# Kernel optimization log

Measured on AMD Instinct MI355X. Metric: run time of the kernel, lower is better.

Reference implementation:

```python
import jax, jax.numpy as jnp
import numpy as np

N = 50000   # nodes
E = 800000  # edges
D = 96      # feature dim


def setup_inputs() -> dict:
    key = jax.random.key(0)
    k1, k2, k3, k4 = jax.random.split(key, 4)
    scale = 1.0 / np.sqrt(D)
    return {
        "x": jax.random.normal(k1, (N, D), dtype=jnp.float32),
        "edge_index": jax.random.randint(k2, (2, E), 0, N, dtype=jnp.int64),
        "W1": jax.random.normal(k3, (D, D), dtype=jnp.float32) * scale,
        "b1": jnp.zeros((D,), dtype=jnp.float32),
        "W2": jax.random.normal(k4, (D, D), dtype=jnp.float32) * scale,
        "b2": jnp.zeros((D,), dtype=jnp.float32),
    }


def _gcn_conv(x, src, dst, W, b, n_nodes):
    # PyG GCNConv: linear transform, add self-loops, symmetric normalization,
    # scatter-add aggregation from src (row) to dst (col), then bias.
    h = x @ W  # [N, D_out]
    loops = jnp.arange(n_nodes, dtype=src.dtype)
    s = jnp.concatenate([src, loops])  # [E+N]
    d = jnp.concatenate([dst, loops])  # [E+N]
    deg = jax.ops.segment_sum(jnp.ones_like(d, dtype=h.dtype), d, num_segments=n_nodes)
    dinv = jnp.where(deg > 0, jax.lax.rsqrt(deg), 0.0)  # deg^-1/2, 0 for isolated
    norm = dinv[s] * dinv[d]  # [E+N]
    msg = norm[:, None] * h[s]  # gather + scale
    out = jax.ops.segment_sum(msg, d, num_segments=n_nodes)  # scatter-add
    return out + b


def reference(x, edge_index, W1, b1, W2, b2):
    src, dst = edge_index[0], edge_index[1]
    # dropout p=0.0 -> identity. ReLU after every layer (loop break never fires).
    h = _gcn_conv(x, src, dst, W1, b1, N)
    h = jax.nn.relu(h)
    h = _gcn_conv(h, src, dst, W2, b2, N)
    h = jax.nn.relu(h)
    return h
```

## Files before the change

kernel.cpp:

```cpp
#include <hip/hip_runtime.h>
#include <hip/hip_fp16.h>

#define NN 50000
#define EE 800000
#define DD 96

#define NBIN 196
#define CE   4096
#define CB   196
#define EPT2 16



__global__ __launch_bounds__(256) void k_hist(const int* __restrict__ ei,
                                              int* __restrict__ histB) {
    __shared__ int hist[NBIN];
    int t = threadIdx.x;
    if (t < NBIN) hist[t] = 0;
    __syncthreads();
    int e0 = blockIdx.x * CE;
#pragma unroll
    for (int k = 0; k < EPT2; ++k) {
        int e = e0 + k * 256 + t;
        if (e < EE) atomicAdd(&hist[ei[EE + e] >> 8], 1);
    }
    __syncthreads();
    if (t < NBIN) histB[t * CB + blockIdx.x] = hist[t];
}


__global__ __launch_bounds__(256) void k_scan_bins(int* __restrict__ histB,
                                                   int* __restrict__ binTot) {
    __shared__ int sh[256];
    int t = threadIdx.x;
    int b = blockIdx.x;
    int v = (t < CB) ? histB[b * CB + t] : 0;
    sh[t] = v;
    __syncthreads();
    for (int off = 1; off < 256; off <<= 1) {
        int u = (t >= off) ? sh[t - off] : 0;
        __syncthreads();
        sh[t] += u;
        __syncthreads();
    }
    if (t < CB) histB[b * CB + t] = sh[t] - v;
    if (t == 255) binTot[b] = sh[255];
}


__global__ __launch_bounds__(256) void k_scan_tot(const int* __restrict__ binTot,
                                                  int* __restrict__ binbase) {
    __shared__ int sh[256];
    int t = threadIdx.x;
    int v = (t < NBIN) ? binTot[t] : 0;
    sh[t] = v;
    __syncthreads();
    for (int off = 1; off < 256; off <<= 1) {
        int u = (t >= off) ? sh[t - off] : 0;
        __syncthreads();
        sh[t] += u;
        __syncthreads();
    }
    if (t < NBIN) binbase[t] = sh[t] - v;
    if (t == 0) binbase[NBIN] = EE;
}


__global__ __launch_bounds__(256) void k_scatter_bins(const int* __restrict__ ei,
                                                      const int* __restrict__ histB,
                                                      const int* __restrict__ binbase,
                                                      int* __restrict__ packed) {
    __shared__ int hist[NBIN];
    __shared__ int lofs[NBIN + 1];
    __shared__ int cur[NBIN];
    __shared__ int sstart[NBIN];
    __shared__ int buf[CE];
    __shared__ int sh[256];
    int t = threadIdx.x;
    int e0 = blockIdx.x * CE;
    int nE = min(CE, EE - e0);

    int s[EPT2], d[EPT2];
#pragma unroll
    for (int k = 0; k < EPT2; ++k) {
        int e = e0 + k * 256 + t;
        s[k] = (e < EE) ? ei[e] : 0;
        d[k] = (e < EE) ? ei[EE + e] : -1;
    }
    if (t < NBIN) hist[t] = 0;
    __syncthreads();
#pragma unroll
    for (int k = 0; k < EPT2; ++k)
        if (d[k] >= 0) atomicAdd(&hist[d[k] >> 8], 1);
    __syncthreads();
    int v = (t < NBIN) ? hist[t] : 0;
    sh[t] = v;
    __syncthreads();
    for (int off = 1; off < 256; off <<= 1) {
        int u = (t >= off) ? sh[t - off] : 0;
        __syncthreads();
        sh[t] += u;
        __syncthreads();
    }
    if (t < NBIN) { lofs[t] = sh[t] - v; cur[t] = sh[t] - v; }
    if (t == 0) lofs[NBIN] = nE;
    if (t < NBIN) sstart[t] = binbase[t] + histB[t * CB + blockIdx.x];
    __syncthreads();
#pragma unroll
    for (int k = 0; k < EPT2; ++k)
        if (d[k] >= 0) {
            int b = d[k] >> 8;
            int pos = atomicAdd(&cur[b], 1);
            buf[pos] = s[k] | ((d[k] & 0xFF) << 16);
        }
    __syncthreads();
    for (int i = t; i < nE; i += 256) {
        int blo = 0, bhi = NBIN;
        while (bhi - blo > 1) {
            int mid = (blo + bhi) >> 1;
            if (lofs[mid] <= i) blo = mid; else bhi = mid;
        }
        packed[sstart[blo] + (i - lofs[blo])] = buf[i];
    }
}


__global__ __launch_bounds__(256) void k_csr(const int* __restrict__ packed,
                                             const int* __restrict__ binbase,
                                             int* __restrict__ rp,
                                             float* __restrict__ dinv,
                                             int* __restrict__ col,
                                             const float* __restrict__ x,
                                             __half* __restrict__ xh) {
    __shared__ int h256[256];
    __shared__ int cur[256];
    __shared__ int sh[256];
    __shared__ float sdinv[256];
    int t = threadIdx.x;
    int b = blockIdx.x;
    int base = binbase[b];
    int nE = binbase[b + 1] - base;

    h256[t] = 0;
    __syncthreads();
    for (int i = t; i < nE; i += 256)
        atomicAdd(&h256[(packed[base + i] >> 16) & 0xFF], 1);
    __syncthreads();
    int v = h256[t];
    sh[t] = v;
    __syncthreads();
    for (int off = 1; off < 256; off <<= 1) {
        int u = (t >= off) ? sh[t - off] : 0;
        __syncthreads();
        sh[t] += u;
        __syncthreads();
    }
    int ex = sh[t] - v;
    cur[t] = ex;
    float di = rsqrtf((float)(v + 1));
    sdinv[t] = di;
    int node = b * 256 + t;
    if (node <= NN) rp[node] = base + ex;
    if (node < NN) dinv[node] = di;
    __syncthreads();
    for (int i = t; i < nE; i += 256) {
        int pv = packed[base + i];
        int pos = atomicAdd(&cur[(pv >> 16) & 0xFF], 1);
        col[base + pos] = pv & 0xFFFF;
    }
    for (int i = t; i < 256 * 12; i += 256) {
        int rr = i / 12;
        int cc = i % 12;
        int r = b * 256 + rr;
        if (r < NN) {
            float sc = sdinv[rr];
            const float4* xx = (const float4*)x + (size_t)r * 24 + cc * 2;
            float4 f0 = xx[0], f1 = xx[1];
            __half h[8];
            h[0] = __float2half_rn(sc * f0.x); h[1] = __float2half_rn(sc * f0.y);
            h[2] = __float2half_rn(sc * f0.z); h[3] = __float2half_rn(sc * f0.w);
            h[4] = __float2half_rn(sc * f1.x); h[5] = __float2half_rn(sc * f1.y);
            h[6] = __float2half_rn(sc * f1.z); h[7] = __float2half_rn(sc * f1.w);
            ((uint4*)xh)[(size_t)r * 12 + cc] = *(uint4*)h;
        }
    }
}


template <int FINAL>
__global__ __launch_bounds__(384) void k_fused(const __half* __restrict__ xh,
                                               const int* __restrict__ rp,
                                               const int* __restrict__ col,
                                               const float* __restrict__ dinv,
                                               const float* __restrict__ W,
                                               const float* __restrict__ b,
                                               __half* __restrict__ acth,
                                               float* __restrict__ outf) {
    __shared__ __half Wl[DD * DD];
    __shared__ float Al[32][100];
    int t = threadIdx.x;
    for (int i = t; i < DD * DD / 8; i += 384) {
        const float4* ww = (const float4*)W;
        float4 f0 = ww[i * 2], f1 = ww[i * 2 + 1];
        __half h[8];
        h[0] = __float2half_rn(f0.x); h[1] = __float2half_rn(f0.y);
        h[2] = __float2half_rn(f0.z); h[3] = __float2half_rn(f0.w);
        h[4] = __float2half_rn(f1.x); h[5] = __float2half_rn(f1.y);
        h[6] = __float2half_rn(f1.z); h[7] = __float2half_rn(f1.w);
        ((uint4*)Wl)[i] = *(uint4*)h;
    }

    int c  = t % 12;
    int ny = t / 12;
    int d = blockIdx.x * 32 + ny;
    const uint4* h4 = (const uint4*)xh;

    if (d < NN) {
        union U { uint4 u; __half2 h[4]; };
        U self; self.u = h4[d * 12 + c];
        float dd = dinv[d];
        int j0 = rp[d], j1 = rp[d + 1];

        float2 aA[4] = {{0,0},{0,0},{0,0},{0,0}};
        float2 aB[4] = {{0,0},{0,0},{0,0},{0,0}};
        int j = j0;
        int n0, n1, n2, n3;
        bool have4 = (j + 3 < j1);
        if (have4) { n0 = col[j]; n1 = col[j+1]; n2 = col[j+2]; n3 = col[j+3]; }
        while (have4) {
            bool next4 = (j + 7 < j1);
            int m0, m1, m2, m3;
            if (next4) {
                m0 = col[j+4]; m1 = col[j+5]; m2 = col[j+6]; m3 = col[j+7];
            }
            U v0, v1, v2, v3;
            v0.u = h4[n0 * 12 + c];
            v1.u = h4[n1 * 12 + c];
            v2.u = h4[n2 * 12 + c];
            v3.u = h4[n3 * 12 + c];
#pragma unroll
            for (int k = 0; k < 4; ++k) {
                float2 f0 = __half22float2(v0.h[k]);
                float2 f1 = __half22float2(v1.h[k]);
                float2 f2 = __half22float2(v2.h[k]);
                float2 f3 = __half22float2(v3.h[k]);
                aA[k].x += f0.x + f1.x; aA[k].y += f0.y + f1.y;
                aB[k].x += f2.x + f3.x; aB[k].y += f2.y + f3.y;
            }
            n0 = m0; n1 = m1; n2 = m2; n3 = m3;
            j += 4;
            have4 = next4;
        }
        for (; j < j1; ++j) {
            U v; v.u = h4[col[j] * 12 + c];
#pragma unroll
            for (int k = 0; k < 4; ++k) {
                float2 f = __half22float2(v.h[k]);
                aA[k].x += f.x; aA[k].y += f.y;
            }
        }
        float v[8];
#pragma unroll
        for (int k = 0; k < 4; ++k) {
            float2 fs = __half22float2(self.h[k]);
            v[2*k]   = dd * (aA[k].x + aB[k].x + fs.x);
            v[2*k+1] = dd * (aA[k].y + aB[k].y + fs.y);
        }
        *(float4*)&Al[ny][c * 8]     = make_float4(v[0], v[1], v[2], v[3]);
        *(float4*)&Al[ny][c * 8 + 4] = make_float4(v[4], v[5], v[6], v[7]);
    }
    __syncthreads();

    int tx = t % 24;
    int ry = t / 24;
    int c0 = tx * 4;
    float a0x = 0.f, a0y = 0.f, a0z = 0.f, a0w = 0.f;
    float a1x = 0.f, a1y = 0.f, a1z = 0.f, a1w = 0.f;
#pragma unroll 8
    for (int k = 0; k < DD; ++k) {
        uint2 wv = *(const uint2*)&Wl[k * DD + c0];
        const __half2* wh = (const __half2*)&wv;
        float2 w01 = __half22float2(wh[0]);
        float2 w23 = __half22float2(wh[1]);
        float r0 = Al[ry][k];
        float r1 = Al[ry + 16][k];
        a0x += r0 * w01.x; a0y += r0 * w01.y; a0z += r0 * w23.x; a0w += r0 * w23.y;
        a1x += r1 * w01.x; a1y += r1 * w01.y; a1z += r1 * w23.x; a1w += r1 * w23.y;
    }
    float4 bb = *(const float4*)&b[c0];
    int g0 = blockIdx.x * 32 + ry;
    int g1 = g0 + 16;
    float r0x = fmaxf(a0x + bb.x, 0.f), r0y = fmaxf(a0y + bb.y, 0.f);
    float r0z = fmaxf(a0z + bb.z, 0.f), r0w = fmaxf(a0w + bb.w, 0.f);
    float r1x = fmaxf(a1x + bb.x, 0.f), r1y = fmaxf(a1y + bb.y, 0.f);
    float r1z = fmaxf(a1z + bb.z, 0.f), r1w = fmaxf(a1w + bb.w, 0.f);
    if (g0 < NN) {
        if (FINAL) {
            *(float4*)&outf[g0 * DD + c0] = make_float4(r0x, r0y, r0z, r0w);
        } else {
            float sc = dinv[g0];
            __half h[4];
            h[0] = __float2half_rn(sc * r0x); h[1] = __float2half_rn(sc * r0y);
            h[2] = __float2half_rn(sc * r0z); h[3] = __float2half_rn(sc * r0w);
            *(uint2*)&acth[g0 * DD + c0] = *(uint2*)h;
        }
    }
    if (g1 < NN) {
        if (FINAL) {
            *(float4*)&outf[g1 * DD + c0] = make_float4(r1x, r1y, r1z, r1w);
        } else {
            float sc = dinv[g1];
            __half h[4];
            h[0] = __float2half_rn(sc * r1x); h[1] = __float2half_rn(sc * r1y);
            h[2] = __float2half_rn(sc * r1z); h[3] = __float2half_rn(sc * r1w);
            *(uint2*)&acth[g1 * DD + c0] = *(uint2*)h;
        }
    }
}


extern "C" void kernel_launch(void* const* d_in, const int* in_sizes, int n_in,
                              void* d_out, int out_size, void* d_ws, size_t ws_size,
                              hipStream_t stream) {
    const float* x  = (const float*)d_in[0];
    const int*   ei = (const int*)d_in[1];
    const float* W1 = (const float*)d_in[2];
    const float* b1 = (const float*)d_in[3];
    const float* W2 = (const float*)d_in[4];
    const float* b2 = (const float*)d_in[5];
    float* out = (float*)d_out;

    char* p = (char*)d_ws;
    int*   histB   = (int*)p;   p += ((size_t)NBIN * CB * 4 + 255) & ~(size_t)255;
    int*   binTot  = (int*)p;   p += ((size_t)NBIN * 4 + 255) & ~(size_t)255;
    int*   binbase = (int*)p;   p += ((size_t)(NBIN + 1) * 4 + 255) & ~(size_t)255;
    int*   rp      = (int*)p;   p += ((size_t)(NN + 1) * 4 + 255) & ~(size_t)255;
    float* dinv    = (float*)p; p += ((size_t)NN * 4 + 255) & ~(size_t)255;
    int*   col     = (int*)p;   p += ((size_t)EE * 4 + 255) & ~(size_t)255;
    __half* bufA   = (__half*)p; p += ((size_t)NN * DD * 2 + 255) & ~(size_t)255;
    __half* bufB   = (__half*)p;
    int*   packed  = (int*)bufB;

    k_hist<<<CB, 256, 0, stream>>>(ei, histB);
    k_scan_bins<<<NBIN, 256, 0, stream>>>(histB, binTot);
    k_scan_tot<<<1, 256, 0, stream>>>(binTot, binbase);
    k_scatter_bins<<<CB, 256, 0, stream>>>(ei, histB, binbase, packed);
    k_csr<<<NBIN, 256, 0, stream>>>(packed, binbase, rp, dinv, col, x, bufA);

    k_fused<0><<<(NN + 31) / 32, 384, 0, stream>>>(bufA, rp, col, dinv, W1, b1,
                                                   bufB, nullptr);

    k_fused<1><<<(NN + 31) / 32, 384, 0, stream>>>(bufB, rp, col, dinv, W2, b2,
                                                   nullptr, out);
}
```

Measured before the change: 136.0 us.

## Sort nodes by descending degree via counting sort to balance aggregation blocks

Builds a degree histogram inside the CSR kernel, scans it, and computes a permutation that orders nodes by descending in-degree, clamped to 64 bins. Both fused GCN layers then process nodes in that order, so each 32-node block holds nodes of similar degree and warps diverge less in the gather loop. It also drops the software-pipelined prefetch of column indices in favour of a simpler 4-wide loop. The cost is three extra small kernel launches, an extra indirection through perm, and scattered output writes.

```diff
diff --git a/kernel.cpp b/kernel.cpp
--- a/kernel.cpp
+++ b/kernel.cpp
@@ -9,6 +9,7 @@
 #define CE   4096
 #define CB   196
 #define EPT2 16
+#define DB   64
 
 
 
@@ -63,6 +64,23 @@
     }
     if (t < NBIN) binbase[t] = sh[t] - v;
     if (t == 0) binbase[NBIN] = EE;
+}
+
+
+__global__ __launch_bounds__(64) void k_scan_tot64(const int* __restrict__ binTotD,
+                                                   int* __restrict__ degBase) {
+    __shared__ int sh[DB];
+    int t = threadIdx.x;
+    int v = binTotD[t];
+    sh[t] = v;
+    __syncthreads();
+    for (int off = 1; off < DB; off <<= 1) {
+        int u = (t >= off) ? sh[t - off] : 0;
+        __syncthreads();
+        sh[t] += u;
+        __syncthreads();
+    }
+    degBase[t] = sh[t] - v;
 }
 
 
@@ -131,17 +149,20 @@
                                              float* __restrict__ dinv,
                                              int* __restrict__ col,
                                              const float* __restrict__ x,
-                                             __half* __restrict__ xh) {
+                                             __half* __restrict__ xh,
+                                             int* __restrict__ histD) {
     __shared__ int h256[256];
     __shared__ int cur[256];
     __shared__ int sh[256];
     __shared__ float sdinv[256];
+    __shared__ int hd[DB];
     int t = threadIdx.x;
     int b = blockIdx.x;
     int base = binbase[b];
     int nE = binbase[b + 1] - base;
 
     h256[t] = 0;
+    if (t < DB) hd[t] = 0;
     __syncthreads();
     for (int i = t; i < nE; i += 256)
         atomicAdd(&h256[(packed[base + i] >> 16) & 0xFF], 1);
@@ -161,8 +182,12 @@
     sdinv[t] = di;
     int node = b * 256 + t;
     if (node <= NN) rp[node] = base + ex;
-    if (node < NN) dinv[node] = di;
-    __syncthreads();
+    if (node < NN) {
+        dinv[node] = di;
+        atomicAdd(&hd[(DB - 1) - min(v, DB - 1)], 1);
+    }
+    __syncthreads();
+    if (t < DB) histD[t * CB + b] = hd[t];
     for (int i = t; i < nE; i += 256) {
         int pv = packed[base + i];
         int pos = atomicAdd(&cur[(pv >> 16) & 0xFF], 1);
@@ -187,11 +212,31 @@
 }
 
 
+__global__ __launch_bounds__(256) void k_perm(const int* __restrict__ rp,
+                                              const int* __restrict__ histD,
+                                              const int* __restrict__ degBase,
+                                              int* __restrict__ perm) {
+    __shared__ int lcur[DB];
+    int t = threadIdx.x;
+    int b = blockIdx.x;
+    if (t < DB) lcur[t] = 0;
+    __syncthreads();
+    int node = b * 256 + t;
+    if (node < NN) {
+        int deg = rp[node + 1] - rp[node];
+        int bin = (DB - 1) - min(deg, DB - 1);
+        int loc = atomicAdd(&lcur[bin], 1);
+        perm[degBase[bin] + histD[bin * CB + b] + loc] = node;
+    }
+}
+
+
 template <int FINAL>
 __global__ __launch_bounds__(384) void k_fused(const __half* __restrict__ xh,
                                                const int* __restrict__ rp,
                                                const int* __restrict__ col,
                                                const float* __restrict__ dinv,
+                                               const int* __restrict__ perm,
                                                const float* __restrict__ W,
                                                const float* __restrict__ b,
                                                __half* __restrict__ acth,
@@ -212,7 +257,8 @@
 
     int c  = t % 12;
     int ny = t / 12;
-    int d = blockIdx.x * 32 + ny;
+    int idx = blockIdx.x * 32 + ny;
+    int d = (idx < NN) ? perm[idx] : NN;
     const uint4* h4 = (const uint4*)xh;
 
     if (d < NN) {
@@ -224,20 +270,13 @@
         float2 aA[4] = {{0,0},{0,0},{0,0},{0,0}};
         float2 aB[4] = {{0,0},{0,0},{0,0},{0,0}};
         int j = j0;
-        int n0, n1, n2, n3;
-        bool have4 = (j + 3 < j1);
-        if (have4) { n0 = col[j]; n1 = col[j+1]; n2 = col[j+2]; n3 = col[j+3]; }
-        while (have4) {
-            bool next4 = (j + 7 < j1);
-            int m0, m1, m2, m3;
-            if (next4) {
-                m0 = col[j+4]; m1 = col[j+5]; m2 = col[j+6]; m3 = col[j+7];
-            }
+        for (; j + 3 < j1; j += 4) {
+            int s0 = col[j], s1 = col[j+1], s2 = col[j+2], s3 = col[j+3];
             U v0, v1, v2, v3;
-            v0.u = h4[n0 * 12 + c];
-            v1.u = h4[n1 * 12 + c];
-            v2.u = h4[n2 * 12 + c];
-            v3.u = h4[n3 * 12 + c];
+            v0.u = h4[s0 * 12 + c];
+            v1.u = h4[s1 * 12 + c];
+            v2.u = h4[s2 * 12 + c];
+            v3.u = h4[s3 * 12 + c];
 #pragma unroll
             for (int k = 0; k < 4; ++k) {
                 float2 f0 = __half22float2(v0.h[k]);
@@ -247,9 +286,6 @@
                 aA[k].x += f0.x + f1.x; aA[k].y += f0.y + f1.y;
                 aB[k].x += f2.x + f3.x; aB[k].y += f2.y + f3.y;
             }
-            n0 = m0; n1 = m1; n2 = m2; n3 = m3;
-            j += 4;
-            have4 = next4;
         }
         for (; j < j1; ++j) {
             U v; v.u = h4[col[j] * 12 + c];
@@ -288,8 +324,10 @@
         a1x += r1 * w01.x; a1y += r1 * w01.y; a1z += r1 * w23.x; a1w += r1 * w23.y;
     }
     float4 bb = *(const float4*)&b[c0];
-    int g0 = blockIdx.x * 32 + ry;
-    int g1 = g0 + 16;
+    int i0 = blockIdx.x * 32 + ry;
+    int i1 = i0 + 16;
+    int g0 = (i0 < NN) ? perm[i0] : NN;
+    int g1 = (i1 < NN) ? perm[i1] : NN;
     float r0x = fmaxf(a0x + bb.x, 0.f), r0y = fmaxf(a0y + bb.y, 0.f);
     float r0z = fmaxf(a0z + bb.z, 0.f), r0w = fmaxf(a0w + bb.w, 0.f);
     float r1x = fmaxf(a1x + bb.x, 0.f), r1y = fmaxf(a1y + bb.y, 0.f);
@@ -337,6 +375,10 @@
     int*   rp      = (int*)p;   p += ((size_t)(NN + 1) * 4 + 255) & ~(size_t)255;
     float* dinv    = (float*)p; p += ((size_t)NN * 4 + 255) & ~(size_t)255;
     int*   col     = (int*)p;   p += ((size_t)EE * 4 + 255) & ~(size_t)255;
+    int*   histD   = (int*)p;   p += ((size_t)DB * CB * 4 + 255) & ~(size_t)255;
+    int*   binTotD = (int*)p;   p += ((size_t)DB * 4 + 255) & ~(size_t)255;
+    int*   degBase = (int*)p;   p += ((size_t)DB * 4 + 255) & ~(size_t)255;
+    int*   perm    = (int*)p;   p += ((size_t)NN * 4 + 255) & ~(size_t)255;
     __half* bufA   = (__half*)p; p += ((size_t)NN * DD * 2 + 255) & ~(size_t)255;
     __half* bufB   = (__half*)p;
     int*   packed  = (int*)bufB;
@@ -345,11 +387,14 @@
     k_scan_bins<<<NBIN, 256, 0, stream>>>(histB, binTot);
     k_scan_tot<<<1, 256, 0, stream>>>(binTot, binbase);
     k_scatter_bins<<<CB, 256, 0, stream>>>(ei, histB, binbase, packed);
-    k_csr<<<NBIN, 256, 0, stream>>>(packed, binbase, rp, dinv, col, x, bufA);
-
-    k_fused<0><<<(NN + 31) / 32, 384, 0, stream>>>(bufA, rp, col, dinv, W1, b1,
-                                                   bufB, nullptr);
-
-    k_fused<1><<<(NN + 31) / 32, 384, 0, stream>>>(bufB, rp, col, dinv, W2, b2,
-                                                   nullptr, out);
-}
+    k_csr<<<NBIN, 256, 0, stream>>>(packed, binbase, rp, dinv, col, x, bufA, histD);
+    k_scan_bins<<<DB, 256, 0, stream>>>(histD, binTotD);
+    k_scan_tot64<<<1, 64, 0, stream>>>(binTotD, degBase);
+    k_perm<<<NBIN, 256, 0, stream>>>(rp, histD, degBase, perm);
+
+    k_fused<0><<<(NN + 31) / 32, 384, 0, stream>>>(bufA, rp, col, dinv, perm,
+                                                   W1, b1, bufB, nullptr);
+
+    k_fused<1><<<(NN + 31) / 32, 384, 0, stream>>>(bufB, rp, col, dinv, perm,
+                                                   W2, b2, nullptr, out);
+}
```

Result: no change. 137.4 us (+1.0%).
